# Kernel tuning notes

Hardware: AMD Instinct MI355X
Metric: run time of the kernel (lower is better)

The kernel has to match this reference:

```python
import jax, jax.numpy as jnp
import numpy as np

T, H, I, E, TOP_K = 2048, 1024, 768, 8, 2


def setup_inputs() -> dict:
    key = jax.random.key(0)
    kx, kg, ku, kd, kr = jax.random.split(key, 5)
    scale_h = 1.0 / np.sqrt(H)
    scale_i = 1.0 / np.sqrt(I)
    x = jax.random.normal(kx, (T, H), dtype=jnp.float32)
    gate_w = jax.random.normal(kg, (E, I, H), dtype=jnp.float32) * scale_h
    up_w = jax.random.normal(ku, (E, I, H), dtype=jnp.float32) * scale_h
    down_w = jax.random.normal(kd, (E, H, I), dtype=jnp.float32) * scale_i
    # Router: top-k over random logits, softmax over selected, scatter to dense [T, E]
    logits = jax.random.normal(kr, (T, E), dtype=jnp.float32)
    top_vals, top_idx = jax.lax.top_k(logits, TOP_K)          # [T, K]
    top_w = jax.nn.softmax(top_vals, axis=-1)                 # [T, K]
    rows = jnp.arange(T)[:, None]                             # [T, 1]
    masked_routing_weights = jnp.zeros((T, E), jnp.float32).at[rows, top_idx].set(top_w)
    expert_select_count = jnp.zeros((E,), jnp.int32).at[top_idx.reshape(-1)].add(1)
    return {
        "x": x,
        "gate_w": gate_w,
        "up_w": up_w,
        "down_w": down_w,
        "masked_routing_weights": masked_routing_weights,
        "expert_select_count": expert_select_count,
    }


def reference(x, gate_w, up_w, down_w, masked_routing_weights, expert_select_count):
    # custom_moe_glu: per-expert GLU MLP, combined with masked routing weights.
    # x: [T, H]; gate_w/up_w: [E, I, H]; down_w: [E, H, I]; routing: [T, E]
    g = jnp.einsum("th,eih->tei", x, gate_w)                  # [T, E, I]
    u = jnp.einsum("th,eih->tei", x, up_w)                    # [T, E, I]
    h = jax.nn.silu(g) * u                                    # fused GLU activation
    # down projection per expert, then weighted combine over experts
    out = jnp.einsum("tei,ehi,te->th", h, down_w, masked_routing_weights)
    return out
```

## Files before the change

kernel.cpp:

```cpp
#include <hip/hip_runtime.h>
#include <hip/hip_bf16.h>

#define T_TOK 2048
#define H_DIM 1024
#define I_DIM 768
#define NEXP  8
#define XSTR  1056
#define WSTR  1056

typedef short bf16x8  __attribute__((ext_vector_type(8)));
typedef short short4v __attribute__((ext_vector_type(4)));
typedef float f32x4   __attribute__((ext_vector_type(4)));

__device__ __forceinline__ short f2bf(float f) {
  __bf16 b = (__bf16)f;
  return __builtin_bit_cast(short, b);
}
__device__ __forceinline__ void gload16(const void* g, void* l) {
  __builtin_amdgcn_global_load_lds(
      (const __attribute__((address_space(1))) void*)g,
      (__attribute__((address_space(3))) void*)l, 16, 0, 0);
}
__device__ __forceinline__ int padcnt(int c) { return (c + 127) & ~127; }
__device__ __forceinline__ int ebase(const int* __restrict__ cnts, int e) {
  int b = 0;
#pragma unroll
  for (int i = 0; i < NEXP; ++i)
    if (i < e) b += padcnt(cnts[i]);
  return b;
}


__global__ __launch_bounds__(512) void compact_k(const float* __restrict__ routw,
                                                 int* __restrict__ wsI) {
  __shared__ int sc[8];
  int e = blockIdx.x, tid = threadIdx.x, lane = tid & 63, w = tid >> 6;
  unsigned long long mk[4];
  int cnt = 0;
#pragma unroll
  for (int c = 0; c < 4; ++c) {
    int tk = w * 256 + c * 64 + lane;
    float v = routw[(size_t)tk * NEXP + e];
    mk[c] = __ballot(v > 0.f);
    cnt += __popcll(mk[c]);
  }
  if (lane == 0) sc[w] = cnt;
  __syncthreads();
  int run = 0, tot = 0;
#pragma unroll
  for (int j = 0; j < 8; ++j) {
    if (j < w) run += sc[j];
    tot += sc[j];
  }
#pragma unroll
  for (int c = 0; c < 4; ++c) {
    int tk = w * 256 + c * 64 + lane;
    if ((mk[c] >> lane) & 1ull) {
      int pos = __popcll(mk[c] & ((1ull << lane) - 1));
      wsI[64 + e * T_TOK + run + pos] = tk;
    }
    run += __popcll(mk[c]);
  }
  if (w == 7 && lane == 0) wsI[e] = tot;
  int pad = padcnt(tot);
  for (int r = tot + tid; r < pad; r += 512) wsI[64 + e * T_TOK + r] = T_TOK;
}

__global__ __launch_bounds__(256) void pre_k(const float* __restrict__ x,
                                             const float* __restrict__ gw,
                                             const float* __restrict__ uw,
                                             const float* __restrict__ dw,
                                             unsigned short* __restrict__ x_bf,
                                             unsigned short* __restrict__ gbf,
                                             unsigned short* __restrict__ ubf,
                                             unsigned short* __restrict__ dbf,
                                             float* __restrict__ out) {
  int bid = blockIdx.x, tid = threadIdx.x;
  int col = (tid & 63) * 16;
  if (bid < 520) {
    int r = bid * 4 + (tid >> 6);
    if (r > 2048) return;
    unsigned short* dst = x_bf + (size_t)r * XSTR + col;
    if (r < 2048) {
      const float* sr = x + (size_t)r * H_DIM + col;
#pragma unroll
      for (int j = 0; j < 4; ++j) {
        float4 v = *(const float4*)(sr + j * 4);
        short4v b = {f2bf(v.x), f2bf(v.y), f2bf(v.z), f2bf(v.w)};
        *(short4v*)(dst + j * 4) = b;
      }
    } else {
#pragma unroll
      for (int j = 0; j < 4; ++j) {
        short4v z = {0, 0, 0, 0};
        *(short4v*)(dst + j * 4) = z;
      }
    }
  } else if (bid < 3592) {
    int a = (bid < 2056) ? 0 : 1;
    int r = (bid - (a ? 2056 : 520)) * 4 + (tid >> 6);
    const float* s = (a ? uw : gw) + (size_t)r * H_DIM + col;
    unsigned short* dst = (a ? ubf : gbf) + (size_t)r * WSTR + col;
#pragma unroll
    for (int j = 0; j < 4; ++j) {
      float4 v = *(const float4*)(s + j * 4);
      short4v b = {f2bf(v.x), f2bf(v.y), f2bf(v.z), f2bf(v.w)};
      *(short4v*)(dst + j * 4) = b;
    }
  } else if (bid < 5128) {
    size_t off = ((size_t)(bid - 3592) * 256 + tid) * 16;
    const float* s = dw + off;
    unsigned short* o = dbf + off;
#pragma unroll
    for (int j = 0; j < 4; ++j) {
      float4 v = *(const float4*)(s + j * 4);
      short4v b = {f2bf(v.x), f2bf(v.y), f2bf(v.z), f2bf(v.w)};
      *(short4v*)(o + j * 4) = b;
    }
  } else {
    size_t off = ((size_t)(bid - 5128) * 256 + tid) * 16;
    f32x4 z = {0.f, 0.f, 0.f, 0.f};
#pragma unroll
    for (int j = 0; j < 4; ++j) *(f32x4*)(out + off + j * 4) = z;
  }
}

#define WB(v)                                              \
  do {                                                     \
    asm volatile("s_waitcnt vmcnt(" #v ")" ::: "memory");  \
    __builtin_amdgcn_s_barrier();                          \
    __builtin_amdgcn_sched_barrier(0);                     \
  } while (0)

__global__ __launch_bounds__(512, 2) void gemm1_k(
    const unsigned short* __restrict__ x_bf, const unsigned short* __restrict__ gbf,
    const unsigned short* __restrict__ ubf, const int* __restrict__ wsI,
    unsigned short* __restrict__ h) {
  int e = blockIdx.x & 7, rr = blockIdx.x >> 3;
  int mt = rr & 15, nt = rr >> 4;
  int cnt = wsI[e];
  int m0 = mt * 128;
  if (m0 >= cnt) return;
  int base = ebase(wsI, e);
  int n0 = nt * 128;

  __shared__ unsigned short ls[5][12288];

  int tid = threadIdx.x, lane = tid & 63, w = tid >> 6;
  int wm = w >> 2, wn = w & 3;
  int fr = lane & 15, fg = lane >> 4;
  int srow = lane >> 2;
  int scol = (((lane & 3) ^ (srow & 3) ^ ((srow >> 2) & 1))) * 8;

  int tokA = wsI[64 + e * T_TOK + m0 + 16 * w + srow];
  const unsigned short* srcA = x_bf + (size_t)tokA * XSTR + scol;
  const unsigned short* srcG = gbf + (size_t)(e * I_DIM + n0 + 16 * w + srow) * WSTR + scol;
  const unsigned short* srcU = ubf + (size_t)(e * I_DIM + n0 + 16 * w + srow) * WSTR + scol;

  int sl = ((fg ^ (fr & 3) ^ ((fr >> 2) & 1)) << 3);
  int roA[4], roB[4];
#pragma unroll
  for (int m = 0; m < 4; ++m) roA[m] = (wm * 64 + m * 16 + fr) * 32 + sl;
#pragma unroll
  for (int n = 0; n < 4; ++n) {
    int r2 = (n < 2) ? (wn * 32 + n * 16 + fr) : (128 + wn * 32 + (n - 2) * 16 + fr);
    roB[n] = 4096 + r2 * 32 + sl;
  }

  bf16x8 af[2][4], bv[2][4];
  f32x4 acc[4][4] = {};

#define STG1(hh)                                                     \
  do {                                                               \
    unsigned short* lb = &ls[(hh) % 5][0];                           \
    gload16(srcA + (hh) * 32, lb + w * 512);                         \
    gload16(srcG + (hh) * 32, lb + 4096 + w * 512);                  \
    gload16(srcU + (hh) * 32, lb + 4096 + (w + 8) * 512);            \
  } while (0)
#define LDF1(st, hh)                                                 \
  do {                                                               \
    const unsigned short* lb = &ls[(hh) % 5][0];                     \
    _Pragma("unroll") for (int m = 0; m < 4; ++m) af[st][m] = *(const bf16x8*)(lb + roA[m]); \
    _Pragma("unroll") for (int n = 0; n < 4; ++n) bv[st][n] = *(const bf16x8*)(lb + roB[n]); \
  } while (0)
#define MM1(st)                                                      \
  do {                                                               \
    __builtin_amdgcn_s_setprio(1);                                   \
    _Pragma("unroll") for (int m = 0; m < 4; ++m)                    \
      _Pragma("unroll") for (int n = 0; n < 4; ++n)                  \
        acc[m][n] = __builtin_amdgcn_mfma_f32_16x16x32_bf16(af[st][m], bv[st][n], acc[m][n], 0, 0, 0); \
    __builtin_amdgcn_s_setprio(0);                                   \
  } while (0)

  STG1(0); STG1(1); STG1(2); STG1(3);
  WB(6);
  LDF1(0, 0);
#pragma unroll
  for (int i = 0; i < 32; ++i) {
    if (i + 4 < 32) STG1(i + 4);
    if (i + 1 < 32) LDF1((i + 1) & 1, i + 1);
    MM1(i & 1);
    if (i <= 27)      WB(6);
    else if (i == 28) WB(3);
    else if (i == 29) WB(0);
  }
#undef STG1
#undef LDF1
#undef MM1

#pragma unroll
  for (int m = 0; m < 4; ++m)
#pragma unroll
    for (int j = 0; j < 4; ++j) {
      int row = wm * 64 + m * 16 + fg * 4 + j;
      size_t rb2 = (size_t)(base + m0 + row) * I_DIM + n0;
#pragma unroll
      for (int jn = 0; jn < 2; ++jn) {
        float g = acc[m][jn][j];
        float u = acc[m][jn + 2][j];
        h[rb2 + wn * 32 + jn * 16 + fr] = (unsigned short)f2bf(g * u / (1.f + __expf(-g)));
      }
    }
}

__global__ __launch_bounds__(512, 2) void gemm2_k(
    const unsigned short* __restrict__ h, const unsigned short* __restrict__ dbf,
    const int* __restrict__ wsI, const float* __restrict__ routw,
    float* __restrict__ out) {
  int e = blockIdx.x & 7, rr = blockIdx.x >> 3;
  int mt = rr & 15, nt = rr >> 4;
  int cnt = wsI[e];
  int m0 = mt * 128;
  if (m0 >= cnt) return;
  int base = ebase(wsI, e);
  int n0 = nt * 256;

  __shared__ unsigned short ls[5][12288];

  int tid = threadIdx.x, lane = tid & 63, w = tid >> 6;
  int wm = w >> 2, wn = w & 3;
  int fr = lane & 15, fg = lane >> 4;
  int srow = lane >> 2;
  int scol = (((lane & 3) ^ (srow & 3) ^ ((srow >> 2) & 1))) * 8;

  const unsigned short* srcA  = h + (size_t)(base + m0 + 16 * w + srow) * I_DIM + scol;
  const unsigned short* srcB1 = dbf + (size_t)(e * H_DIM + n0 + 16 * w + srow) * I_DIM + scol;
  const unsigned short* srcB2 = dbf + (size_t)(e * H_DIM + n0 + 16 * (w + 8) + srow) * I_DIM + scol;

  int sl = ((fg ^ (fr & 3) ^ ((fr >> 2) & 1)) << 3);
  int roA[4], roB[4];
#pragma unroll
  for (int m = 0; m < 4; ++m) roA[m] = (wm * 64 + m * 16 + fr) * 32 + sl;
#pragma unroll
  for (int n = 0; n < 4; ++n) roB[n] = 4096 + (wn * 64 + n * 16 + fr) * 32 + sl;

  bf16x8 af[2][4], bv[2][4];
  f32x4 acc[4][4] = {};

#define STG2(hh)                                                     \
  do {                                                               \
    unsigned short* lb = &ls[(hh) % 5][0];                           \
    gload16(srcA + (hh) * 32, lb + w * 512);                         \
    gload16(srcB1 + (hh) * 32, lb + 4096 + w * 512);                 \
    gload16(srcB2 + (hh) * 32, lb + 4096 + (w + 8) * 512);           \
  } while (0)
#define LDF2(st, hh)                                                 \
  do {                                                               \
    const unsigned short* lb = &ls[(hh) % 5][0];                     \
    _Pragma("unroll") for (int m = 0; m < 4; ++m) af[st][m] = *(const bf16x8*)(lb + roA[m]); \
    _Pragma("unroll") for (int n = 0; n < 4; ++n) bv[st][n] = *(const bf16x8*)(lb + roB[n]); \
  } while (0)
#define MM2(st)                                                      \
  do {                                                               \
    __builtin_amdgcn_s_setprio(1);                                   \
    _Pragma("unroll") for (int m = 0; m < 4; ++m)                    \
      _Pragma("unroll") for (int n = 0; n < 4; ++n)                  \
        acc[m][n] = __builtin_amdgcn_mfma_f32_16x16x32_bf16(af[st][m], bv[st][n], acc[m][n], 0, 0, 0); \
    __builtin_amdgcn_s_setprio(0);                                   \
  } while (0)

  STG2(0); STG2(1); STG2(2); STG2(3);
  WB(6);
  LDF2(0, 0);
#pragma unroll
  for (int i = 0; i < 24; ++i) {
    if (i + 4 < 24) STG2(i + 4);
    if (i + 1 < 24) LDF2((i + 1) & 1, i + 1);
    MM2(i & 1);
    if (i <= 19)      WB(6);
    else if (i == 20) WB(3);
    else if (i == 21) WB(0);
  }
#undef STG2
#undef LDF2
#undef MM2

#pragma unroll
  for (int m = 0; m < 4; ++m)
#pragma unroll
    for (int j = 0; j < 4; ++j) {
      int row = wm * 64 + m * 16 + fg * 4 + j;
      int grow = m0 + row;
      if (grow < cnt) {
        int tk = wsI[64 + e * T_TOK + grow];
        float rw = routw[(size_t)tk * NEXP + e];
        float* orow = out + (size_t)tk * H_DIM + n0 + wn * 64;
#pragma unroll
        for (int n = 0; n < 4; ++n)
          atomicAdd(orow + n * 16 + fr, acc[m][n][j] * rw);
      }
    }
}

extern "C" void kernel_launch(void* const* d_in, const int* in_sizes, int n_in,
                              void* d_out, int out_size, void* d_ws, size_t ws_size,
                              hipStream_t stream) {
  const float* x      = (const float*)d_in[0];
  const float* gate_w = (const float*)d_in[1];
  const float* up_w   = (const float*)d_in[2];
  const float* down_w = (const float*)d_in[3];
  const float* routw  = (const float*)d_in[4];
  float* out = (float*)d_out;
  int* wsI = (int*)d_ws;

  unsigned short* x_bf = (unsigned short*)((char*)d_ws + 131072);
  unsigned short* gbf  = (unsigned short*)((char*)d_ws + 4458560);
  unsigned short* ubf  = (unsigned short*)((char*)d_ws + 17434688);
  unsigned short* dbf  = (unsigned short*)((char*)d_ws + 30410816);
  unsigned short* h    = (unsigned short*)((char*)d_ws + 42993728);

  compact_k<<<8, 512, 0, stream>>>(routw, wsI);
  pre_k<<<5640, 256, 0, stream>>>(x, gate_w, up_w, down_w, x_bf, gbf, ubf, dbf, out);
  gemm1_k<<<768, 512, 0, stream>>>(x_bf, gbf, ubf, wsI, h);
  gemm2_k<<<512, 512, 0, stream>>>(h, dbf, wsI, routw, out);
}
```

Before: 91.60 us.

## Retile gate/up GEMM to 64x64 blocks and use nontemporal stores in conversion

The fused gate/up GEMM kernel is rewritten with 256-thread blocks on 64-token by 64-column tiles and a simple double-buffered LDS pipeline, replacing the 128x128 tiles with a 5-stage buffer. Per-expert padding is reduced from 128 to 64 rows. With the routed token counts, the old grid left many CUs idle, and smaller tiles give more active blocks and less padded work. The precision-conversion and zeroing stores become nontemporal. In exchange, the shallower pipeline and smaller tiles give less data reuse per block. The smaller padding may also interact with the 128-row tiles of the down-projection kernel.

```diff
diff --git a/kernel.cpp b/kernel.cpp
--- a/kernel.cpp
+++ b/kernel.cpp
@@ -21,7 +21,13 @@
       (const __attribute__((address_space(1))) void*)g,
       (__attribute__((address_space(3))) void*)l, 16, 0, 0);
 }
-__device__ __forceinline__ int padcnt(int c) { return (c + 127) & ~127; }
+__device__ __forceinline__ void ntst(unsigned short* p, short4v v) {
+  __builtin_nontemporal_store(v, (short4v*)p);
+}
+__device__ __forceinline__ void ntstf(float* p, f32x4 v) {
+  __builtin_nontemporal_store(v, (f32x4*)p);
+}
+__device__ __forceinline__ int padcnt(int c) { return (c + 63) & ~63; }
 __device__ __forceinline__ int ebase(const int* __restrict__ cnts, int e) {
   int b = 0;
 #pragma unroll
@@ -87,14 +93,12 @@
       for (int j = 0; j < 4; ++j) {
         float4 v = *(const float4*)(sr + j * 4);
         short4v b = {f2bf(v.x), f2bf(v.y), f2bf(v.z), f2bf(v.w)};
-        *(short4v*)(dst + j * 4) = b;
+        ntst(dst + j * 4, b);
       }
     } else {
-#pragma unroll
-      for (int j = 0; j < 4; ++j) {
-        short4v z = {0, 0, 0, 0};
-        *(short4v*)(dst + j * 4) = z;
-      }
+      short4v z = {0, 0, 0, 0};
+#pragma unroll
+      for (int j = 0; j < 4; ++j) ntst(dst + j * 4, z);
     }
   } else if (bid < 3592) {
     int a = (bid < 2056) ? 0 : 1;
@@ -105,7 +109,7 @@
     for (int j = 0; j < 4; ++j) {
       float4 v = *(const float4*)(s + j * 4);
       short4v b = {f2bf(v.x), f2bf(v.y), f2bf(v.z), f2bf(v.w)};
-      *(short4v*)(dst + j * 4) = b;
+      ntst(dst + j * 4, b);
     }
   } else if (bid < 5128) {
     size_t off = ((size_t)(bid - 3592) * 256 + tid) * 16;
@@ -115,14 +119,98 @@
     for (int j = 0; j < 4; ++j) {
       float4 v = *(const float4*)(s + j * 4);
       short4v b = {f2bf(v.x), f2bf(v.y), f2bf(v.z), f2bf(v.w)};
-      *(short4v*)(o + j * 4) = b;
+      ntst(o + j * 4, b);
     }
   } else {
     size_t off = ((size_t)(bid - 5128) * 256 + tid) * 16;
     f32x4 z = {0.f, 0.f, 0.f, 0.f};
 #pragma unroll
-    for (int j = 0; j < 4; ++j) *(f32x4*)(out + off + j * 4) = z;
-  }
+    for (int j = 0; j < 4; ++j) ntstf(out + off + j * 4, z);
+  }
+}
+
+__global__ __launch_bounds__(256, 4) void gemm1_k(
+    const unsigned short* __restrict__ x_bf, const unsigned short* __restrict__ gbf,
+    const unsigned short* __restrict__ ubf, const int* __restrict__ wsI,
+    unsigned short* __restrict__ h) {
+  int e = blockIdx.x & 7, rr = blockIdx.x >> 3;
+  int mt = rr & 31, ng = rr >> 5;
+  int cnt = wsI[e];
+  int m0 = mt * 64;
+  if (m0 >= cnt) return;
+  int base = ebase(wsI, e);
+  int g0 = ng * 64;
+
+  __shared__ unsigned short ls[2][6144];
+
+  int tid = threadIdx.x, lane = tid & 63, w = tid >> 6;
+  int wm = w >> 1, wn = w & 1;
+  int fr = lane & 15, fg = lane >> 4;
+  int srow = lane >> 2;
+  int scol = ((lane & 3) ^ (srow & 3) ^ ((srow >> 2) & 1)) * 8;
+
+  const unsigned short* src[3];
+  int ldo[3];
+  {
+    int tok = wsI[64 + e * T_TOK + m0 + 16 * w + srow];
+    src[0] = x_bf + (size_t)tok * XSTR + scol;
+    ldo[0] = w * 512;
+    src[1] = gbf + (size_t)(e * I_DIM + g0 + 16 * w + srow) * WSTR + scol;
+    ldo[1] = (w + 4) * 512;
+    src[2] = ubf + (size_t)(e * I_DIM + g0 + 16 * w + srow) * WSTR + scol;
+    ldo[2] = (w + 8) * 512;
+  }
+
+  int sl = ((fg ^ (fr & 3) ^ ((fr >> 2) & 1)) << 3);
+  int roA[2], roB[4];
+#pragma unroll
+  for (int m = 0; m < 2; ++m) roA[m] = (wm * 32 + m * 16 + fr) * 32 + sl;
+#pragma unroll
+  for (int n = 0; n < 4; ++n) {
+    int r2 = (n < 2) ? (wn * 32 + n * 16 + fr) : (64 + wn * 32 + (n - 2) * 16 + fr);
+    roB[n] = 2048 + r2 * 32 + sl;
+  }
+
+  f32x4 acc[2][4] = {};
+
+#define STG1(buf, k)                                                 \
+  do {                                                               \
+    _Pragma("unroll") for (int i = 0; i < 3; ++i)                    \
+      gload16(src[i] + (k) * 32, &ls[buf][ldo[i]]);                  \
+  } while (0)
+
+  STG1(0, 0);
+  __syncthreads();
+  for (int k = 0; k < 32; ++k) {
+    int cur = k & 1;
+    if (k + 1 < 32) STG1(cur ^ 1, k + 1);
+    bf16x8 af[2], bv[4];
+#pragma unroll
+    for (int m = 0; m < 2; ++m) af[m] = *(const bf16x8*)&ls[cur][roA[m]];
+#pragma unroll
+    for (int n = 0; n < 4; ++n) bv[n] = *(const bf16x8*)&ls[cur][roB[n]];
+#pragma unroll
+    for (int m = 0; m < 2; ++m)
+#pragma unroll
+      for (int n = 0; n < 4; ++n)
+        acc[m][n] = __builtin_amdgcn_mfma_f32_16x16x32_bf16(af[m], bv[n], acc[m][n], 0, 0, 0);
+    __syncthreads();
+  }
+#undef STG1
+
+#pragma unroll
+  for (int m = 0; m < 2; ++m)
+#pragma unroll
+    for (int j = 0; j < 4; ++j) {
+      int row = wm * 32 + m * 16 + fg * 4 + j;
+      size_t rb2 = (size_t)(base + m0 + row) * I_DIM + g0;
+#pragma unroll
+      for (int jn = 0; jn < 2; ++jn) {
+        float g = acc[m][jn][j];
+        float u = acc[m][jn + 2][j];
+        h[rb2 + wn * 32 + jn * 16 + fr] = (unsigned short)f2bf(g * u / (1.f + __expf(-g)));
+      }
+    }
 }
 
 #define WB(v)                                              \
@@ -131,97 +219,6 @@
     __builtin_amdgcn_s_barrier();                          \
     __builtin_amdgcn_sched_barrier(0);                     \
   } while (0)
-
-__global__ __launch_bounds__(512, 2) void gemm1_k(
-    const unsigned short* __restrict__ x_bf, const unsigned short* __restrict__ gbf,
-    const unsigned short* __restrict__ ubf, const int* __restrict__ wsI,
-    unsigned short* __restrict__ h) {
-  int e = blockIdx.x & 7, rr = blockIdx.x >> 3;
-  int mt = rr & 15, nt = rr >> 4;
-  int cnt = wsI[e];
-  int m0 = mt * 128;
-  if (m0 >= cnt) return;
-  int base = ebase(wsI, e);
-  int n0 = nt * 128;
-
-  __shared__ unsigned short ls[5][12288];
-
-  int tid = threadIdx.x, lane = tid & 63, w = tid >> 6;
-  int wm = w >> 2, wn = w & 3;
-  int fr = lane & 15, fg = lane >> 4;
-  int srow = lane >> 2;
-  int scol = (((lane & 3) ^ (srow & 3) ^ ((srow >> 2) & 1))) * 8;
-
-  int tokA = wsI[64 + e * T_TOK + m0 + 16 * w + srow];
-  const unsigned short* srcA = x_bf + (size_t)tokA * XSTR + scol;
-  const unsigned short* srcG = gbf + (size_t)(e * I_DIM + n0 + 16 * w + srow) * WSTR + scol;
-  const unsigned short* srcU = ubf + (size_t)(e * I_DIM + n0 + 16 * w + srow) * WSTR + scol;
-
-  int sl = ((fg ^ (fr & 3) ^ ((fr >> 2) & 1)) << 3);
-  int roA[4], roB[4];
-#pragma unroll
-  for (int m = 0; m < 4; ++m) roA[m] = (wm * 64 + m * 16 + fr) * 32 + sl;
-#pragma unroll
-  for (int n = 0; n < 4; ++n) {
-    int r2 = (n < 2) ? (wn * 32 + n * 16 + fr) : (128 + wn * 32 + (n - 2) * 16 + fr);
-    roB[n] = 4096 + r2 * 32 + sl;
-  }
-
-  bf16x8 af[2][4], bv[2][4];
-  f32x4 acc[4][4] = {};
-
-#define STG1(hh)                                                     \
-  do {                                                               \
-    unsigned short* lb = &ls[(hh) % 5][0];                           \
-    gload16(srcA + (hh) * 32, lb + w * 512);                         \
-    gload16(srcG + (hh) * 32, lb + 4096 + w * 512);                  \
-    gload16(srcU + (hh) * 32, lb + 4096 + (w + 8) * 512);            \
-  } while (0)
-#define LDF1(st, hh)                                                 \
-  do {                                                               \
-    const unsigned short* lb = &ls[(hh) % 5][0];                     \
-    _Pragma("unroll") for (int m = 0; m < 4; ++m) af[st][m] = *(const bf16x8*)(lb + roA[m]); \
-    _Pragma("unroll") for (int n = 0; n < 4; ++n) bv[st][n] = *(const bf16x8*)(lb + roB[n]); \
-  } while (0)
-#define MM1(st)                                                      \
-  do {                                                               \
-    __builtin_amdgcn_s_setprio(1);                                   \
-    _Pragma("unroll") for (int m = 0; m < 4; ++m)                    \
-      _Pragma("unroll") for (int n = 0; n < 4; ++n)                  \
-        acc[m][n] = __builtin_amdgcn_mfma_f32_16x16x32_bf16(af[st][m], bv[st][n], acc[m][n], 0, 0, 0); \
-    __builtin_amdgcn_s_setprio(0);                                   \
-  } while (0)
-
-  STG1(0); STG1(1); STG1(2); STG1(3);
-  WB(6);
-  LDF1(0, 0);
-#pragma unroll
-  for (int i = 0; i < 32; ++i) {
-    if (i + 4 < 32) STG1(i + 4);
-    if (i + 1 < 32) LDF1((i + 1) & 1, i + 1);
-    MM1(i & 1);
-    if (i <= 27)      WB(6);
-    else if (i == 28) WB(3);
-    else if (i == 29) WB(0);
-  }
-#undef STG1
-#undef LDF1
-#undef MM1
-
-#pragma unroll
-  for (int m = 0; m < 4; ++m)
-#pragma unroll
-    for (int j = 0; j < 4; ++j) {
-      int row = wm * 64 + m * 16 + fg * 4 + j;
-      size_t rb2 = (size_t)(base + m0 + row) * I_DIM + n0;
-#pragma unroll
-      for (int jn = 0; jn < 2; ++jn) {
-        float g = acc[m][jn][j];
-        float u = acc[m][jn + 2][j];
-        h[rb2 + wn * 32 + jn * 16 + fr] = (unsigned short)f2bf(g * u / (1.f + __expf(-g)));
-      }
-    }
-}
 
 __global__ __launch_bounds__(512, 2) void gemm2_k(
     const unsigned short* __restrict__ h, const unsigned short* __restrict__ dbf,
@@ -331,6 +328,6 @@
 
   compact_k<<<8, 512, 0, stream>>>(routw, wsI);
   pre_k<<<5640, 256, 0, stream>>>(x, gate_w, up_w, down_w, x_bf, gbf, ubf, dbf, out);
-  gemm1_k<<<768, 512, 0, stream>>>(x_bf, gbf, ubf, wsI, h);
+  gemm1_k<<<3072, 256, 0, stream>>>(x_bf, gbf, ubf, wsI, h);
   gemm2_k<<<512, 512, 0, stream>>>(h, dbf, wsI, routw, out);
 }
```

Result: slower. 126.5 us (+38.1%).
